# Kernel optimization log

Hardware: AMD Instinct MI355X
Metric: run time of the kernel (lower is better)

The kernel has to match this reference:

```python
import jax, jax.numpy as jnp
import numpy as np

NUM_EXPERTS = 64
TOP_K = 6
ALPHA = 1e-3
HIDDEN = 128


def setup_inputs() -> dict:
    key = jax.random.key(0)
    k1, k2 = jax.random.split(key)
    hidden_states = jax.random.normal(k1, (64, 4096, HIDDEN), dtype=jnp.float32)
    # kaiming_uniform_(a=sqrt(5)) on weight of shape (64, 128): bound = 1/sqrt(fan_in)
    bound = 1.0 / np.sqrt(HIDDEN)
    W = jax.random.uniform(k2, (NUM_EXPERTS, HIDDEN), dtype=jnp.float32, minval=-bound, maxval=bound)
    return {"hidden_states": hidden_states, "W": W}


def reference(hidden_states, W):
    b, s, h = hidden_states.shape
    x = hidden_states.reshape(-1, h)                      # (N, h)
    logits = x @ W.T                                      # (N, 64)
    scores = jax.nn.softmax(logits, axis=-1)
    topk_weight, topk_idx = jax.lax.top_k(scores, TOP_K)  # (N, 6)
    # norm_topk_prob=True
    topk_weight = topk_weight / (topk_weight.sum(-1, keepdims=True) + 1e-20)
    # aux loss (training path, seq_aux=False): ce = one_hot(topk_idx).mean(0)
    counts = jnp.zeros(NUM_EXPERTS, dtype=scores.dtype).at[topk_idx.ravel()].add(1.0)
    ce = counts / jnp.asarray(topk_idx.size, scores.dtype)
    Pi = scores.mean(0)
    fi = ce * NUM_EXPERTS
    aux_loss = (Pi * fi).sum() * ALPHA
    return topk_idx, topk_weight, aux_loss
```

## Files before the change

### kernel.cpp

```cpp
#include <hip/hip_runtime.h>
#include <cfloat>

#define NTOK (64 * 4096)
#define HID  128
#define NE   64
#define TK   6
#define TS   7
#define BLK  256
#define TPB  256
#define GRID (NTOK / TPB)
#define KSCALE 131072.0f
#define KINV   (1.0f / 131072.0f)
#define KTHR   1664

typedef __attribute__((ext_vector_type(8))) short short8;
typedef __attribute__((ext_vector_type(4))) float f32x4;

union UB { uint4 u; short8 s; };
__device__ __forceinline__ short8 u2s(const uint4 u) { UB x; x.u = u; return x.s; }
__device__ __forceinline__ int imax(int a, int b) { return a > b ? a : b; }
__device__ __forceinline__ int imin(int a, int b) { return a < b ? a : b; }

__device__ __forceinline__ void split2(float a, float b, unsigned& d1, unsigned& d2) {
    unsigned p1;
    asm("v_cvt_pk_bf16_f32 %0, %1, %2" : "=v"(p1) : "v"(a), "v"(b));
    const float a1 = __uint_as_float(p1 << 16);
    const float b1 = __uint_as_float(p1 & 0xFFFF0000u);
    const float ra = a - a1;
    const float rb = b - b1;
    unsigned p2;
    asm("v_cvt_pk_bf16_f32 %0, %1, %2" : "=v"(p2) : "v"(ra), "v"(rb));
    d1 = p1; d2 = p2;
}

__device__ __forceinline__ void split8(const float4 v0, const float4 v1,
                                       uint4& o1, uint4& o2) {
    split2(v0.x, v0.y, o1.x, o2.x);
    split2(v0.z, v0.w, o1.y, o2.y);
    split2(v1.x, v1.y, o1.z, o2.z);
    split2(v1.z, v1.w, o1.w, o2.w);
}

__global__ __launch_bounds__(BLK)
void gate_kernel(const float* __restrict__ X,
                 const float* __restrict__ W,
                 float* __restrict__ oidx,
                 float* __restrict__ ow,
                 float* __restrict__ Pi_g,
                 unsigned int* __restrict__ cnt_g)
{
    __shared__ uint4        Wlds[2 * 1024];
    __shared__ float        Pi_s[4][NE];
    __shared__ unsigned int cnt_s[NE];
    __shared__ unsigned int flags_s[TPB];
    __shared__ unsigned int nflag_s;

    const int tid  = threadIdx.x;
    const int lane = tid & 63;
    const int wv   = __builtin_amdgcn_readfirstlane(tid >> 6);
    const int col  = lane & 15;
    const int g    = lane >> 4;

    if (tid < NE) cnt_s[tid] = 0u;
    if (tid == 0) nflag_s = 0u;

    {
        const float4* W4 = (const float4*)W;
#pragma unroll
        for (int i = 0; i < 4; ++i) {
            const int slot = tid + i * BLK;
            const int fid  = slot >> 6;
            const int ln   = slot & 63;
            const int e    = ((fid >> 2) << 4) + (ln & 15);
            const int kq   = ((fid & 3) << 3) + ((ln >> 4) << 1);
            const float4 v0 = W4[e * 32 + kq];
            const float4 v1 = W4[e * 32 + kq + 1];
            uint4 o1, o2;
            split8(v0, v1, o1, o2);
            Wlds[slot]        = o1;
            Wlds[1024 + slot] = o2;
        }
    }
    __syncthreads();

    const int tok0 = blockIdx.x * TPB + wv * 64;

    f32x4 acc[4][4];
#pragma unroll
    for (int tt = 0; tt < 4; ++tt)
#pragma unroll
        for (int et = 0; et < 4; ++et) acc[tt][et] = (f32x4)0.0f;

#pragma unroll
    for (int kt = 0; kt < 4; ++kt) {
        uint4 xs[2][4];
#pragma unroll
        for (int tt = 0; tt < 4; ++tt) {
            const float4* xp = (const float4*)(X + (size_t)(tok0 + tt * 16 + col) * HID)
                               + (kt * 8 + g * 2);
            split8(xp[0], xp[1], xs[0][tt], xs[1][tt]);
        }
#pragma unroll
        for (int et = 0; et < 4; ++et) {
            const int fb = ((et << 2) + kt) * 64 + lane;
            const short8 w1 = u2s(Wlds[fb]);
            const short8 w2 = u2s(Wlds[1024 + fb]);
#define MM4(WF, XI) { \
            acc[0][et] = __builtin_amdgcn_mfma_f32_16x16x32_bf16(WF, u2s(xs[XI][0]), acc[0][et], 0, 0, 0); \
            acc[1][et] = __builtin_amdgcn_mfma_f32_16x16x32_bf16(WF, u2s(xs[XI][1]), acc[1][et], 0, 0, 0); \
            acc[2][et] = __builtin_amdgcn_mfma_f32_16x16x32_bf16(WF, u2s(xs[XI][2]), acc[2][et], 0, 0, 0); \
            acc[3][et] = __builtin_amdgcn_mfma_f32_16x16x32_bf16(WF, u2s(xs[XI][3]), acc[3][et], 0, 0, 0); }
            MM4(w1, 0) MM4(w1, 1) MM4(w2, 0) MM4(w2, 1)
#undef MM4
        }
    }

    float pi[16];
#pragma unroll
    for (int j = 0; j < 16; ++j) pi[j] = 0.0f;

#pragma unroll
    for (int tt = 0; tt < 4; ++tt) {
        int tv[TS];
#pragma unroll
        for (int q = 0; q < TS; ++q) tv[q] = (int)0x80000000;
#pragma unroll
        for (int j = 0; j < 16; ++j) {
            const float f = acc[tt][j >> 2][j & 3];
            const int  ik = (int)(f * KSCALE);
            const int   e = ((j >> 2) << 4) + (g << 2) + (j & 3);
            int m = (int)(((unsigned)ik << 6) | (unsigned)(63 - e));
#pragma unroll
            for (int q = 0; q < TS; ++q) {
                const int t = tv[q];
                tv[q] = imax(t, m);
                m     = imin(t, m);
            }
        }
        const float ml = (float)(tv[0] >> 6) * KINV;
        float Zl = 0.0f;
#pragma unroll
        for (int j = 0; j < 16; ++j) {
            const float e = __expf(acc[tt][j >> 2][j & 3] - ml);
            acc[tt][j >> 2][j & 3] = e;
            Zl += e;
        }
        float m_self = ml, Z = Zl;
#pragma unroll
        for (int lv = 16; lv <= 32; lv <<= 1) {
            int rv[TS];
#pragma unroll
            for (int q = 0; q < TS; ++q) rv[q] = __shfl_xor(tv[q], lv);
            const float m_p = (float)(rv[0] >> 6) * KINV;
            const float Z_p = __shfl_xor(Z, lv);
#pragma unroll
            for (int q2 = 0; q2 < TS; ++q2) {
                int m = rv[q2];
#pragma unroll
                for (int q = 0; q < TS; ++q) {
                    const int t = tv[q];
                    tv[q] = imax(t, m);
                    m     = imin(t, m);
                }
            }
            const float m_n = (float)(tv[0] >> 6) * KINV;
            Z = Z * __expf(m_self - m_n) + Z_p * __expf(m_p - m_n);
            m_self = m_n;
        }
        const float mx  = (float)(tv[0] >> 6) * KINV;
        const float rzt = 1.0f / Z;
        float ex[TK]; float s = 0.0f;
#pragma unroll
        for (int q = 0; q < TK; ++q) {
            ex[q] = __expf((float)(tv[q] >> 6) * KINV - mx);
            s += ex[q];
        }
        const float rs = 1.0f / (s + 1e-20f);
        if (g == tt) {
            bool flag = false;
#pragma unroll
            for (int q = 0; q < TK; ++q) flag |= (tv[q] - tv[q + 1]) < KTHR;
            int te[TK];
#pragma unroll
            for (int q = 0; q < TK; ++q) te[q] = 63 - (tv[q] & 63);
            const size_t gt = (size_t)(tok0 + lane) * TK;
            float2* ip = (float2*)(oidx + gt);
            float2* wp = (float2*)(ow + gt);
            ip[0] = make_float2((float)te[0], (float)te[1]);
            ip[1] = make_float2((float)te[2], (float)te[3]);
            ip[2] = make_float2((float)te[4], (float)te[5]);
            wp[0] = make_float2(ex[0] * rs, ex[1] * rs);
            wp[1] = make_float2(ex[2] * rs, ex[3] * rs);
            wp[2] = make_float2(ex[4] * rs, ex[5] * rs);
            if (!flag) {
#pragma unroll
                for (int q = 0; q < TK; ++q) atomicAdd(&cnt_s[te[q]], 1u);
            } else {
                const unsigned slot = atomicAdd(&nflag_s, 1u);
                flags_s[slot] = (unsigned)(wv * 64 + lane);
            }
        }
        const float sc = __expf(ml - mx) * rzt;
#pragma unroll
        for (int j = 0; j < 16; ++j)
            pi[j] = fmaf(acc[tt][j >> 2][j & 3], sc, pi[j]);
    }

#pragma unroll
    for (int sh = 1; sh <= 8; sh <<= 1)
#pragma unroll
        for (int j = 0; j < 16; ++j) pi[j] += __shfl_xor(pi[j], sh);
    if (col == 0) {
#pragma unroll
        for (int j = 0; j < 16; ++j)
            Pi_s[wv][((j >> 2) << 4) + (g << 2) + (j & 3)] = pi[j];
    }
    __syncthreads();

    {
        const int nf = (int)nflag_s;
        for (int i = wv; i < nf; i += 4) {
            const int tl = (int)flags_s[i];
            const float4* xr = (const float4*)(X + (size_t)(blockIdx.x * TPB + tl) * HID);
            const float4* wr = (const float4*)(W + (size_t)lane * HID);
            float a = 0.0f;
#pragma unroll 8
            for (int kq = 0; kq < 32; ++kq) {
                const float4 xv = xr[kq];
                const float4 wv4 = wr[kq];
                a = fmaf(xv.x, wv4.x, a);
                a = fmaf(xv.y, wv4.y, a);
                a = fmaf(xv.z, wv4.z, a);
                a = fmaf(xv.w, wv4.w, a);
            }
            float tv[TK]; int ti[TK];
#pragma unroll
            for (int q = 0; q < TK; ++q) { tv[q] = -FLT_MAX; ti[q] = 0; }
            for (int e = 0; e < NE; ++e) {
                float m = __shfl(a, e);
                int  mi = e;
#pragma unroll
                for (int q = 0; q < TK; ++q) {
                    const bool  cx = m > tv[q];
                    const float nt = cx ? m     : tv[q];
                    const float nm = cx ? tv[q] : m;
                    const int   ni = cx ? mi    : ti[q];
                    const int   nj = cx ? ti[q] : mi;
                    tv[q] = nt; m = nm; ti[q] = ni; mi = nj;
                }
            }
            const float mx = tv[0];
            float ex[TK]; float s = 0.0f;
#pragma unroll
            for (int q = 0; q < TK; ++q) { ex[q] = __expf(tv[q] - mx); s += ex[q]; }
            const float rs = 1.0f / (s + 1e-20f);
            if (lane == 0) {
                const size_t gt = (size_t)(blockIdx.x * TPB + tl) * TK;
                float2* ip = (float2*)(oidx + gt);
                float2* wp = (float2*)(ow + gt);
                ip[0] = make_float2((float)ti[0], (float)ti[1]);
                ip[1] = make_float2((float)ti[2], (float)ti[3]);
                ip[2] = make_float2((float)ti[4], (float)ti[5]);
                wp[0] = make_float2(ex[0] * rs, ex[1] * rs);
                wp[1] = make_float2(ex[2] * rs, ex[3] * rs);
                wp[2] = make_float2(ex[4] * rs, ex[5] * rs);
#pragma unroll
                for (int q = 0; q < TK; ++q) atomicAdd(&cnt_s[ti[q]], 1u);
            }
        }
    }
    __syncthreads();

    if (tid < NE) {
        atomicAdd(&Pi_g[tid], Pi_s[0][tid] + Pi_s[1][tid] + Pi_s[2][tid] + Pi_s[3][tid]);
        atomicAdd(&cnt_g[tid], cnt_s[tid]);
    }
}

__global__ void aux_kernel(const float* __restrict__ Pi_g,
                           const unsigned int* __restrict__ cnt_g,
                           float* __restrict__ out_aux)
{
    const int e = threadIdx.x;
    const float Pi = Pi_g[e] * (1.0f / (float)NTOK);
    const float ce = (float)cnt_g[e] * (1.0f / (float)(NTOK * TK));
    float v = Pi * ce * (float)NE;
#pragma unroll
    for (int off = 32; off > 0; off >>= 1) v += __shfl_down(v, off);
    if (e == 0) out_aux[0] = v * 1.0e-3f;
}

extern "C" void kernel_launch(void* const* d_in, const int* in_sizes, int n_in,
                              void* d_out, int out_size, void* d_ws, size_t ws_size,
                              hipStream_t stream) {
    const float* X = (const float*)d_in[0];
    const float* W = (const float*)d_in[1];

    float* out  = (float*)d_out;
    float* oidx = out;
    float* ow   = out + (size_t)NTOK * TK;
    float* aux  = out + (size_t)NTOK * TK * 2;

    float*        Pi_g  = (float*)d_ws;
    unsigned int* cnt_g = (unsigned int*)((char*)d_ws + 256);

    hipMemsetAsync(d_ws, 0, 512, stream);
    gate_kernel<<<GRID, BLK, 0, stream>>>(X, W, oidx, ow, Pi_g, cnt_g);
    aux_kernel<<<1, 64, 0, stream>>>(Pi_g, cnt_g, aux);
}
```

Before: 249.7 us.

## Transpose logits through LDS so each thread does full per-token top-k

The MFMA accumulators are staged into a padded shared-memory tile so that each thread owns one token's full 64 logits. Top-k, softmax normalisation and output writes then run per thread, and the cross-lane shuffle merges of partial top-7 lists are dropped. Per-expert Pi sums are recomputed from LDS, with each wave covering 16 experts. This adds roughly 67KB of LDS per block, which may lower occupancy, plus extra LDS traffic, barriers and a second pass of exps.

```diff
diff --git a/kernel.cpp b/kernel.cpp
--- a/kernel.cpp
+++ b/kernel.cpp
@@ -9,6 +9,7 @@
 #define BLK  256
 #define TPB  256
 #define GRID (NTOK / TPB)
+#define LST  67
 #define KSCALE 131072.0f
 #define KINV   (1.0f / 131072.0f)
 #define KTHR   1664
@@ -49,17 +50,21 @@
                  float* __restrict__ Pi_g,
                  unsigned int* __restrict__ cnt_g)
 {
-    __shared__ uint4        Wlds[2 * 1024];
-    __shared__ float        Pi_s[4][NE];
+    __shared__ __align__(16) float smem[TPB * LST];
+    __shared__ float        mz[2 * TPB];
+    __shared__ float        Pi_s[NE];
     __shared__ unsigned int cnt_s[NE];
     __shared__ unsigned int flags_s[TPB];
     __shared__ unsigned int nflag_s;
+
+    uint4* Wlds = (uint4*)smem;
 
     const int tid  = threadIdx.x;
     const int lane = tid & 63;
     const int wv   = __builtin_amdgcn_readfirstlane(tid >> 6);
     const int col  = lane & 15;
     const int g    = lane >> 4;
+    const int eb   = wv * 16;
 
     if (tid < NE) cnt_s[tid] = 0u;
     if (tid == 0) nflag_s = 0u;
@@ -115,60 +120,42 @@
         }
     }
 
-    float pi[16];
-#pragma unroll
-    for (int j = 0; j < 16; ++j) pi[j] = 0.0f;
+    __syncthreads();
 
 #pragma unroll
     for (int tt = 0; tt < 4; ++tt) {
+        const int trow = (wv * 64 + tt * 16 + col) * LST;
+#pragma unroll
+        for (int et = 0; et < 4; ++et) {
+            float* p = &smem[trow + et * 16 + g * 4];
+            p[0] = acc[tt][et][0];
+            p[1] = acc[tt][et][1];
+            p[2] = acc[tt][et][2];
+            p[3] = acc[tt][et][3];
+        }
+    }
+    __syncthreads();
+
+    {
+        const int t = tid;
+        const float* Lrow = &smem[t * LST];
         int tv[TS];
 #pragma unroll
         for (int q = 0; q < TS; ++q) tv[q] = (int)0x80000000;
-#pragma unroll
-        for (int j = 0; j < 16; ++j) {
-            const float f = acc[tt][j >> 2][j & 3];
-            const int  ik = (int)(f * KSCALE);
-            const int   e = ((j >> 2) << 4) + (g << 2) + (j & 3);
-            int m = (int)(((unsigned)ik << 6) | (unsigned)(63 - e));
+
+#pragma unroll 8
+        for (int e = 0; e < NE; ++e) {
+            const float f = Lrow[e];
+            int m = (int)(((unsigned)((int)(f * KSCALE)) << 6) | (unsigned)(63 - e));
 #pragma unroll
             for (int q = 0; q < TS; ++q) {
-                const int t = tv[q];
-                tv[q] = imax(t, m);
-                m     = imin(t, m);
+                const int c = tv[q];
+                tv[q] = imax(c, m);
+                m     = imin(c, m);
             }
         }
-        const float ml = (float)(tv[0] >> 6) * KINV;
-        float Zl = 0.0f;
-#pragma unroll
-        for (int j = 0; j < 16; ++j) {
-            const float e = __expf(acc[tt][j >> 2][j & 3] - ml);
-            acc[tt][j >> 2][j & 3] = e;
-            Zl += e;
-        }
-        float m_self = ml, Z = Zl;
-#pragma unroll
-        for (int lv = 16; lv <= 32; lv <<= 1) {
-            int rv[TS];
-#pragma unroll
-            for (int q = 0; q < TS; ++q) rv[q] = __shfl_xor(tv[q], lv);
-            const float m_p = (float)(rv[0] >> 6) * KINV;
-            const float Z_p = __shfl_xor(Z, lv);
-#pragma unroll
-            for (int q2 = 0; q2 < TS; ++q2) {
-                int m = rv[q2];
-#pragma unroll
-                for (int q = 0; q < TS; ++q) {
-                    const int t = tv[q];
-                    tv[q] = imax(t, m);
-                    m     = imin(t, m);
-                }
-            }
-            const float m_n = (float)(tv[0] >> 6) * KINV;
-            Z = Z * __expf(m_self - m_n) + Z_p * __expf(m_p - m_n);
-            m_self = m_n;
-        }
-        const float mx  = (float)(tv[0] >> 6) * KINV;
-        const float rzt = 1.0f / Z;
+
+        const float mx = (float)(tv[0] >> 6) * KINV;
         float ex[TK]; float s = 0.0f;
 #pragma unroll
         for (int q = 0; q < TK; ++q) {
@@ -176,44 +163,59 @@
             s += ex[q];
         }
         const float rs = 1.0f / (s + 1e-20f);
-        if (g == tt) {
-            bool flag = false;
-#pragma unroll
-            for (int q = 0; q < TK; ++q) flag |= (tv[q] - tv[q + 1]) < KTHR;
-            int te[TK];
-#pragma unroll
-            for (int q = 0; q < TK; ++q) te[q] = 63 - (tv[q] & 63);
-            const size_t gt = (size_t)(tok0 + lane) * TK;
-            float2* ip = (float2*)(oidx + gt);
-            float2* wp = (float2*)(ow + gt);
-            ip[0] = make_float2((float)te[0], (float)te[1]);
-            ip[1] = make_float2((float)te[2], (float)te[3]);
-            ip[2] = make_float2((float)te[4], (float)te[5]);
-            wp[0] = make_float2(ex[0] * rs, ex[1] * rs);
-            wp[1] = make_float2(ex[2] * rs, ex[3] * rs);
-            wp[2] = make_float2(ex[4] * rs, ex[5] * rs);
-            if (!flag) {
-#pragma unroll
-                for (int q = 0; q < TK; ++q) atomicAdd(&cnt_s[te[q]], 1u);
-            } else {
-                const unsigned slot = atomicAdd(&nflag_s, 1u);
-                flags_s[slot] = (unsigned)(wv * 64 + lane);
-            }
-        }
-        const float sc = __expf(ml - mx) * rzt;
-#pragma unroll
-        for (int j = 0; j < 16; ++j)
-            pi[j] = fmaf(acc[tt][j >> 2][j & 3], sc, pi[j]);
-    }
-
-#pragma unroll
-    for (int sh = 1; sh <= 8; sh <<= 1)
-#pragma unroll
-        for (int j = 0; j < 16; ++j) pi[j] += __shfl_xor(pi[j], sh);
-    if (col == 0) {
-#pragma unroll
-        for (int j = 0; j < 16; ++j)
-            Pi_s[wv][((j >> 2) << 4) + (g << 2) + (j & 3)] = pi[j];
+        int te[TK];
+#pragma unroll
+        for (int q = 0; q < TK; ++q) te[q] = 63 - (tv[q] & 63);
+
+        const size_t gt = (size_t)(blockIdx.x * TPB + t) * TK;
+        float2* ip = (float2*)(oidx + gt);
+        float2* wp = (float2*)(ow + gt);
+        ip[0] = make_float2((float)te[0], (float)te[1]);
+        ip[1] = make_float2((float)te[2], (float)te[3]);
+        ip[2] = make_float2((float)te[4], (float)te[5]);
+        wp[0] = make_float2(ex[0] * rs, ex[1] * rs);
+        wp[1] = make_float2(ex[2] * rs, ex[3] * rs);
+        wp[2] = make_float2(ex[4] * rs, ex[5] * rs);
+
+        bool flag = false;
+#pragma unroll
+        for (int q = 0; q < TK; ++q) flag |= (tv[q] - tv[q + 1]) < KTHR;
+        if (!flag) {
+#pragma unroll
+            for (int q = 0; q < TK; ++q) atomicAdd(&cnt_s[te[q]], 1u);
+        } else {
+            const unsigned slot = atomicAdd(&nflag_s, 1u);
+            flags_s[slot] = (unsigned)t;
+        }
+
+        float Z = 0.0f;
+#pragma unroll 8
+        for (int e = 0; e < NE; ++e) Z += __expf(Lrow[e] - mx);
+        mz[2*t]     = mx;
+        mz[2*t + 1] = 1.0f / Z;
+    }
+    __syncthreads();
+
+    {
+        float pi[16];
+#pragma unroll
+        for (int j = 0; j < 16; ++j) pi[j] = 0.0f;
+#pragma unroll
+        for (int gg = 0; gg < 4; ++gg) {
+            const int t = lane + 64 * gg;
+            const float mxt = mz[2*t];
+            const float rzt = mz[2*t + 1];
+            const float* p = &smem[t * LST + eb];
+#pragma unroll
+            for (int j = 0; j < 16; ++j)
+                pi[j] += __expf(p[j] - mxt) * rzt;
+        }
+#pragma unroll
+        for (int s = 1; s <= 32; s <<= 1) {
+#pragma unroll
+            for (int j = 0; j < 16; ++j) pi[j] += __shfl_xor(pi[j], s);
+        }
+        if (lane < 16) Pi_s[eb + lane] = pi[lane];
     }
     __syncthreads();
 
@@ -272,7 +274,7 @@
     __syncthreads();
 
     if (tid < NE) {
-        atomicAdd(&Pi_g[tid], Pi_s[0][tid] + Pi_s[1][tid] + Pi_s[2][tid] + Pi_s[3][tid]);
+        atomicAdd(&Pi_g[tid], Pi_s[tid]);
         atomicAdd(&cnt_g[tid], cnt_s[tid]);
     }
 }
```

Result: no change. 245.1 us (-1.8%).
